# Performance work log

Measured on AMD Instinct MI355X. Metric: run time of the kernel, lower is better.

The kernel has to match this reference:

```python
import jax, jax.numpy as jnp
import numpy as np

B, S, DM = 1, 4096, 2048
H, HD = 16, 128
TS = 16          # tile_size
TOPK = 16        # anchor tiles per query
NUM_TILES = S // TS


def setup_inputs() -> dict:
    key = jax.random.key(0)
    ks = jax.random.split(key, 7)
    x = jax.random.normal(ks[0], (B, S, DM), jnp.float32)
    Wq = jax.random.normal(ks[1], (DM, H * HD), jnp.float32) * 0.02
    Wk = jax.random.normal(ks[2], (DM, H * HD), jnp.float32) * 0.02
    Wv = jax.random.normal(ks[3], (DM, H * HD), jnp.float32) * 0.02
    Wo = jax.random.normal(ks[4], (H * HD, DM), jnp.float32) * 0.02
    # RoPE angles: pos * inv_freq, shape [S, HD//2] (= freqs_cis angle)
    inv_freq = 1.0 / (10000.0 ** (np.arange(0, HD, 2, dtype=np.float32) / HD))
    freqs = jnp.asarray(np.arange(S, dtype=np.float32)[:, None] * inv_freq[None, :])
    anchor_indices = jax.random.randint(ks[5], (B, H, S, TOPK), 0, NUM_TILES).astype(jnp.int32)
    return {"x": x, "Wq": Wq, "Wk": Wk, "Wv": Wv, "Wo": Wo,
            "freqs": freqs, "anchor_indices": anchor_indices}


def _rotate_half(z):
    half = z.shape[-1] // 2
    return jnp.concatenate([-z[..., half:], z[..., :half]], axis=-1)


def reference(x, Wq, Wk, Wv, Wo, freqs, anchor_indices):
    b, s, _ = x.shape
    num_tiles = s // TS
    # QKV projections -> [B, H, S, HD]
    q = (x @ Wq).reshape(b, s, H, HD).transpose(0, 2, 1, 3)
    k = (x @ Wk).reshape(b, s, H, HD).transpose(0, 2, 1, 3)
    v = (x @ Wv).reshape(b, s, H, HD).transpose(0, 2, 1, 3)
    # RoPE (half-split / rotate_half convention), float32
    cos = jnp.cos(freqs)[None, None, :s, :]
    sin = jnp.sin(freqs)[None, None, :s, :]
    cos_full = jnp.concatenate([cos, cos], axis=-1)
    sin_full = jnp.concatenate([sin, sin], axis=-1)
    q = q * cos_full + _rotate_half(q) * sin_full
    k = k * cos_full + _rotate_half(k) * sin_full
    # Per-query tile indices: anchor tiles + local tile
    local_tiles = (jnp.arange(s) // TS).astype(jnp.int32)
    local = jnp.broadcast_to(local_tiles[None, None, :, None], (b, H, s, 1))
    tiles = jnp.concatenate([anchor_indices, local], axis=-1)  # [B,H,S,K+1]
    # Representative query per tile (last token of each query tile)
    tile_repr = jnp.arange(TS - 1, s, TS)
    tile_sel = tiles[:, :, tile_repr, :]                        # [B,H,T,K+1]
    # Expand tile indices to token indices
    offsets = jnp.arange(TS)
    token_idx = tile_sel[..., None] * TS + offsets              # [B,H,T,K+1,TS]
    sparse_len = tile_sel.shape[-1] * TS
    flat_idx = jnp.clip(token_idx.reshape(b, H, num_tiles, sparse_len), 0, s - 1)
    # Gather sparse K/V per (batch, head, query-tile)
    k_flat = k.reshape(b * H, s, HD)
    v_flat = v.reshape(b * H, s, HD)
    idx_flat = flat_idx.reshape(b * H, num_tiles, sparse_len)
    k_sparse = jax.vmap(lambda kv, idx: kv[idx])(k_flat, idx_flat)
    v_sparse = jax.vmap(lambda kv, idx: kv[idx])(v_flat, idx_flat)
    k_sparse = k_sparse.reshape(b, H, num_tiles, sparse_len, HD)
    v_sparse = v_sparse.reshape(b, H, num_tiles, sparse_len, HD)
    # Block-sparse attention per tile
    q_tiled = q.reshape(b, H, num_tiles, TS, HD)
    logits = jnp.einsum('bhtqd,bhtkd->bhtqk', q_tiled, k_sparse) / jnp.sqrt(HD)
    q_pos = jnp.arange(s).reshape(num_tiles, TS)
    future_mask = flat_idx[:, :, :, None, :] > q_pos[None, None, :, :, None]
    logits = jnp.where(future_mask, -1e10, logits)
    weights = jax.nn.softmax(logits, axis=-1)
    all_masked = jnp.all(future_mask, axis=-1, keepdims=True)
    weights = jnp.where(all_masked, 0.0, weights)
    weights = jnp.where(jnp.isnan(weights), 0.0, weights)
    out = jnp.einsum('bhtqk,bhtkd->bhtqd', weights, v_sparse)
    out = out.reshape(b, H, s, HD).transpose(0, 2, 1, 3).reshape(b, s, H * HD)
    return out @ Wo
```

## Files before the change

### kernel.cpp

```cpp
#include <hip/hip_runtime.h>

typedef unsigned short u16;
typedef unsigned int u32;
typedef __attribute__((ext_vector_type(8))) short bf16x8;
typedef __attribute__((ext_vector_type(4))) float f32x4;

__device__ __forceinline__ u16 f2bf(float f) {
  union { float f; u32 u; } v; v.f = f;
  u32 u = v.u;
  return (u16)((u + 0x7FFFu + ((u >> 16) & 1u)) >> 16);
}
__device__ __forceinline__ float bf2f(u16 s) {
  union { u32 u; float f; } v; v.u = ((u32)s) << 16;
  return v.f;
}

__device__ __forceinline__ void async16(const void* g, void* l) {
  __builtin_amdgcn_global_load_lds(
      (__attribute__((address_space(1))) void*)g,
      (__attribute__((address_space(3))) void*)l, 16, 0, 0);
}

__global__ void prep1_kernel(const float* __restrict__ x,
                             const float* __restrict__ W0, const float* __restrict__ W1,
                             const float* __restrict__ W2, const float* __restrict__ W3,
                             const float* __restrict__ freqs,
                             u16* __restrict__ xbf, u16* __restrict__ wqkvT,
                             u16* __restrict__ woT,
                             float* __restrict__ ct, float* __restrict__ st) {
  __shared__ float tile[32][33];
  const int bid = blockIdx.x;
  const int tid = threadIdx.x;
  if (bid < 16384) {
    const int z = bid >> 12;
    const float* in = z == 0 ? W0 : z == 1 ? W1 : z == 2 ? W2 : W3;
    u16* out = z == 3 ? woT : wqkvT + (size_t)z * 4194304;
    const int local = bid & 4095;
    const int c0 = (local & 63) * 32, r0 = (local >> 6) * 32;
    const int tx = tid & 31, ty = tid >> 5;
#pragma unroll
    for (int i = ty; i < 32; i += 8) tile[i][tx] = in[(size_t)(r0 + i) * 2048 + c0 + tx];
    __syncthreads();
#pragma unroll
    for (int i = ty; i < 32; i += 8)
      out[(size_t)(c0 + i) * 2048 + r0 + tx] = f2bf(tile[tx][i]);
  } else if (bid < 24576) {
    int i = (bid - 16384) * 256 + tid;
    float4 v = ((const float4*)x)[i];
    ushort4 o;
    o.x = f2bf(v.x); o.y = f2bf(v.y); o.z = f2bf(v.z); o.w = f2bf(v.w);
    ((ushort4*)xbf)[i] = o;
  } else {
    int i = (bid - 24576) * 256 + tid;
    float f = freqs[i];
    ct[i] = cosf(f); st[i] = sinf(f);
  }
}

__global__ void prep2_kernel(u16* __restrict__ q, const u16* __restrict__ k,
                             u16* __restrict__ Kp,
                             const u16* __restrict__ Vin, u16* __restrict__ VT2,
                             const float* __restrict__ ct, const float* __restrict__ st) {
  __shared__ u16 lv[64][132];
  const int bid = blockIdx.x;
  const int tid = threadIdx.x;
  if (bid < 8192) {
    int i = bid * 256 + tid;
    int dp = (i & 31) * 2;
    int hh = (i >> 5) & 15;
    int s  = i >> 9;
    float c0 = ct[s * 64 + dp], c1 = ct[s * 64 + dp + 1];
    float s0 = st[s * 64 + dp], s1 = st[s * 64 + dp + 1];
    size_t base = (size_t)s * 2048 + hh * 128 + dp;
    {
      u32 lo = *(u32*)(q + base);
      u32 hi = *(u32*)(q + base + 64);
      float a0 = bf2f((u16)lo), a1 = bf2f((u16)(lo >> 16));
      float b0 = bf2f((u16)hi), b1 = bf2f((u16)(hi >> 16));
      u32 nlo = (u32)f2bf(a0 * c0 - b0 * s0) | ((u32)f2bf(a1 * c1 - b1 * s1) << 16);
      u32 nhi = (u32)f2bf(b0 * c0 + a0 * s0) | ((u32)f2bf(b1 * c1 + a1 * s1) << 16);
      *(u32*)(q + base) = nlo;
      *(u32*)(q + base + 64) = nhi;
    }
    {
      u32 lo = *(const u32*)(k + base);
      u32 hi = *(const u32*)(k + base + 64);
      float a0 = bf2f((u16)lo), a1 = bf2f((u16)(lo >> 16));
      float b0 = bf2f((u16)hi), b1 = bf2f((u16)(hi >> 16));
      u32 nlo = (u32)f2bf(a0 * c0 - b0 * s0) | ((u32)f2bf(a1 * c1 - b1 * s1) << 16);
      u32 nhi = (u32)f2bf(b0 * c0 + a0 * s0) | ((u32)f2bf(b1 * c1 + a1 * s1) << 16);
      size_t kpb = ((size_t)hh * 4096 + s) * 128 + dp;
      *(u32*)(Kp + kpb) = nlo;
      *(u32*)(Kp + kpb + 64) = nhi;
    }
  } else {
    const int local = bid - 8192;
    const int h = local >> 6;
    const int s0 = (local & 63) * 64;
#pragma unroll
    for (int i = 0; i < 16; ++i) {
      int idx = i * 256 + tid;
      int r = idx >> 6;
      int d2 = idx & 63;
      u32 vv = ((const u32*)Vin)[(size_t)(s0 + r) * 1024 + h * 64 + d2];
      *(u32*)(&lv[r][d2 * 2]) = vv;
    }
    __syncthreads();
#pragma unroll
    for (int i = 0; i < 16; ++i) {
      int idx = i * 256 + tid;
      int k2 = idx & 7;
      int d  = (idx >> 3) & 127;
      int tl = idx >> 10;
      u32 lo = lv[tl * 16 + k2 * 2][d];
      u32 hi = lv[tl * 16 + k2 * 2 + 1][d];
      ((u32*)VT2)[(((size_t)h * 256 + (s0 >> 4) + tl) * 128 + d) * 8 + k2] = lo | (hi << 16);
    }
  }
}

template <int MODE>
__launch_bounds__(256, 2)
__global__ void gemm128_kernel(const u16* __restrict__ A, const u16* __restrict__ Bt,
                               void* __restrict__ C, u16* __restrict__ D1, u16* __restrict__ D2,
                               int M, int N, int K) {
  __shared__ __align__(16) u16 As[128 * 64];
  __shared__ __align__(16) u16 Bs[128 * 64];
  const int tid  = threadIdx.x;
  const int lane = tid & 63;
  const int wave = tid >> 6;
  const int wr = wave >> 1, wc = wave & 1;
  const int brow = blockIdx.y * 128;
  const int bcol = blockIdx.x * 128;

  int a_goff[4], b_goff[4], l_off[4];
#pragma unroll
  for (int i = 0; i < 4; ++i) {
    int p = (wave * 4 + i) * 1024 + lane * 16;
    int row = p >> 7;
    int colb = (p & 127) ^ ((row & 7) << 4);
    a_goff[i] = (brow + row) * K + (colb >> 1);
    b_goff[i] = (bcol + row) * K + (colb >> 1);
    l_off[i] = p;
  }

  f32x4 acc[4][4];
#pragma unroll
  for (int m = 0; m < 4; ++m)
#pragma unroll
    for (int n = 0; n < 4; ++n) acc[m][n] = (f32x4){0.f, 0.f, 0.f, 0.f};

  for (int k0 = 0; k0 < K; k0 += 64) {
#pragma unroll
    for (int i = 0; i < 4; ++i) {
      async16(A + a_goff[i] + k0, (char*)As + l_off[i]);
      async16(Bt + b_goff[i] + k0, (char*)Bs + l_off[i]);
    }
    __syncthreads();
#pragma unroll
    for (int kk = 0; kk < 2; ++kk) {
      bf16x8 af[4], bfr[4];
#pragma unroll
      for (int m = 0; m < 4; ++m) {
        int row = wr * 64 + m * 16 + (lane & 15);
        int byte = (row << 7) + ((kk * 64 + ((lane >> 4) << 4)) ^ ((row & 7) << 4));
        af[m] = *(const bf16x8*)((const char*)As + byte);
      }
#pragma unroll
      for (int n = 0; n < 4; ++n) {
        int row = wc * 64 + n * 16 + (lane & 15);
        int byte = (row << 7) + ((kk * 64 + ((lane >> 4) << 4)) ^ ((row & 7) << 4));
        bfr[n] = *(const bf16x8*)((const char*)Bs + byte);
      }
#pragma unroll
      for (int m = 0; m < 4; ++m)
#pragma unroll
        for (int n = 0; n < 4; ++n)
          acc[m][n] = __builtin_amdgcn_mfma_f32_16x16x32_bf16(af[m], bfr[n], acc[m][n], 0, 0, 0);
    }
    __syncthreads();
  }

  const int r0 = brow + wr * 64;
  const int c0 = bcol + wc * 64;
  if (MODE == 2) {
    const int sel = bcol >> 11;
    u16* dst = sel == 0 ? (u16*)C : sel == 1 ? D1 : D2;
    const int c0l = (bcol & 2047) + wc * 64;
#pragma unroll
    for (int m = 0; m < 4; ++m)
#pragma unroll
      for (int n = 0; n < 4; ++n)
#pragma unroll
        for (int r = 0; r < 4; ++r) {
          int rr = r0 + m * 16 + ((lane >> 4) << 2) + r;
          int cc = c0l + n * 16 + (lane & 15);
          dst[(size_t)rr * 2048 + cc] = f2bf(acc[m][n][r]);
        }
  } else {
#pragma unroll
    for (int m = 0; m < 4; ++m)
#pragma unroll
      for (int n = 0; n < 4; ++n)
#pragma unroll
        for (int r = 0; r < 4; ++r) {
          int rr = r0 + m * 16 + ((lane >> 4) << 2) + r;
          int cc = c0 + n * 16 + (lane & 15);
          if (MODE == 1) ((u16*)C)[(size_t)rr * N + cc] = f2bf(acc[m][n][r]);
          else           ((float*)C)[(size_t)rr * N + cc] = acc[m][n][r];
        }
  }
}

__launch_bounds__(256, 6)
__global__ void attn_kernel(const u16* __restrict__ Q, const u16* __restrict__ Kp,
                            const u16* __restrict__ VT2, const int* __restrict__ anchors,
                            u16* __restrict__ Out) {
  const int t = blockIdx.x;
  const int h = blockIdx.y;
  __shared__ int tiles[20];
  __shared__ __align__(16) float lg[16][292];
  const int tid  = threadIdx.x;
  const int lane = tid & 63;
  const int wave = tid >> 6;
  const int g = lane >> 4;
  const int c = lane & 15;

  if (tid < 16) tiles[tid] = anchors[(size_t)((h << 12) + (t * 16 + 15)) * 16 + tid];
  if (tid == 16) tiles[16] = t;
  if (tid >= 17 && tid < 20) tiles[tid] = 0;
  __syncthreads();

  {
    const u16* qbase = Q + (size_t)(t * 16 + c) * 2048 + h * 128 + g * 8;
    bf16x8 qf[4];
#pragma unroll
    for (int ks = 0; ks < 4; ++ks) qf[ks] = *(const bf16x8*)(qbase + ks * 32);

    int tok_[5];
    const u16* kb_[5];
#pragma unroll
    for (int i = 0; i < 5; ++i) {
      int j = wave + 4 * i;
      tok_[i] = tiles[j] * 16 + c;
      kb_[i] = Kp + ((size_t)h * 4096 + tok_[i]) * 128 + g * 8;
    }
    bf16x8 kfp[2][4];
#pragma unroll
    for (int ks = 0; ks < 4; ++ks) kfp[0][ks] = *(const bf16x8*)(kb_[0] + ks * 32);
#pragma unroll
    for (int i = 0; i < 5; ++i) {
      if (i < 4) {
#pragma unroll
        for (int ks = 0; ks < 4; ++ks)
          kfp[(i + 1) & 1][ks] = *(const bf16x8*)(kb_[i + 1] + ks * 32);
      }
      f32x4 a = (f32x4){0.f, 0.f, 0.f, 0.f};
#pragma unroll
      for (int ks = 0; ks < 4; ++ks)
        a = __builtin_amdgcn_mfma_f32_16x16x32_bf16(qf[ks], kfp[i & 1][ks], a, 0, 0, 0);
      int j = wave + 4 * i;
      if (j < 17) {
#pragma unroll
        for (int r = 0; r < 4; ++r) {
          int qrow = g * 4 + r;
          float vv = a[r] * 0.088388347648318447f;
          if (tok_[i] > t * 16 + qrow) vv = -1e10f;
          lg[qrow][j * 16 + c] = vv;
        }
      }
    }
  }
  __syncthreads();

  {
    const int r = tid >> 4, cc = tid & 15;
    float vals[17];
    float mx = -3.0e38f;
#pragma unroll
    for (int i = 0; i < 17; ++i) { vals[i] = lg[r][i * 16 + cc]; mx = fmaxf(mx, vals[i]); }
#pragma unroll
    for (int d = 1; d < 16; d <<= 1) mx = fmaxf(mx, __shfl_xor(mx, d, 64));
    float sum = 0.f;
#pragma unroll
    for (int i = 0; i < 17; ++i) { vals[i] = __expf(vals[i] - mx); sum += vals[i]; }
#pragma unroll
    for (int d = 1; d < 16; d <<= 1) sum += __shfl_xor(sum, d, 64);
    float inv = sum > 0.f ? 1.0f / sum : 0.f;
    u16* wrow = (u16*)&lg[r][0];
#pragma unroll
    for (int i = 0; i < 17; ++i) wrow[i * 16 + cc] = f2bf(vals[i] * inv);
    wrow[272 + cc] = 0;
  }
  __syncthreads();

  {
    f32x4 o0 = (f32x4){0.f, 0.f, 0.f, 0.f}, o1 = o0;
    const int d0 = wave * 32;
    const size_t hb = (size_t)h * 256;
    const int keyin = (g & 1) * 8;
    const u16* wrow = (const u16*)&lg[c][0];
    const u16* vb_[9];
#pragma unroll
    for (int ks = 0; ks < 9; ++ks) vb_[ks] = VT2 + (hb + tiles[2 * ks + (g >> 1)]) * 2048;
    bf16x8 pb0[2], pb1[2];
    pb0[0] = *(const bf16x8*)(vb_[0] + (d0 + c) * 16 + keyin);
    pb1[0] = *(const bf16x8*)(vb_[0] + (d0 + 16 + c) * 16 + keyin);
#pragma unroll
    for (int ks = 0; ks < 9; ++ks) {
      if (ks < 8) {
        pb0[(ks + 1) & 1] = *(const bf16x8*)(vb_[ks + 1] + (d0 + c) * 16 + keyin);
        pb1[(ks + 1) & 1] = *(const bf16x8*)(vb_[ks + 1] + (d0 + 16 + c) * 16 + keyin);
      }
      bf16x8 af = *(const bf16x8*)(wrow + ks * 32 + g * 8);
      o0 = __builtin_amdgcn_mfma_f32_16x16x32_bf16(af, pb0[ks & 1], o0, 0, 0, 0);
      o1 = __builtin_amdgcn_mfma_f32_16x16x32_bf16(af, pb1[ks & 1], o1, 0, 0, 0);
    }
#pragma unroll
    for (int r = 0; r < 4; ++r) {
      int qrow = g * 4 + r;
      size_t base = (size_t)(t * 16 + qrow) * 2048 + h * 128;
      Out[base + d0 + c]      = f2bf(o0[r]);
      Out[base + d0 + 16 + c] = f2bf(o1[r]);
    }
  }
}

extern "C" void kernel_launch(void* const* d_in, const int* in_sizes, int n_in,
                              void* d_out, int out_size, void* d_ws, size_t ws_size,
                              hipStream_t stream) {
  (void)in_sizes; (void)n_in; (void)out_size; (void)ws_size;
  const float* x      = (const float*)d_in[0];
  const float* Wq     = (const float*)d_in[1];
  const float* Wk     = (const float*)d_in[2];
  const float* Wv     = (const float*)d_in[3];
  const float* Wo     = (const float*)d_in[4];
  const float* freqs  = (const float*)d_in[5];
  const int* anchors  = (const int*)d_in[6];
  float* out = (float*)d_out;

  char* ws = (char*)d_ws;
  const size_t MB = 1024 * 1024;
  u16* xbf   = (u16*)(ws + 0);
  u16* wqkvT = (u16*)(ws + 16 * MB);
  u16* woT   = (u16*)(ws + 40 * MB);
  u16* qbf   = (u16*)(ws + 48 * MB);
  u16* kbf   = (u16*)(ws + 64 * MB);
  u16* vbf   = (u16*)(ws + 80 * MB);
  u16* attnb = (u16*)(ws + 0);
  u16* Kp    = (u16*)(ws + 16 * MB);
  u16* VT2   = (u16*)(ws + 64 * MB);
  float* ct  = (float*)(ws + 96 * MB);
  float* st  = (float*)(ws + 97 * MB);

  prep1_kernel<<<25600, 256, 0, stream>>>(x, Wq, Wk, Wv, Wo, freqs,
                                          xbf, wqkvT, woT, ct, st);
  gemm128_kernel<2><<<dim3(48, 32), 256, 0, stream>>>(xbf, wqkvT, qbf, kbf, vbf,
                                                      4096, 6144, 2048);
  prep2_kernel<<<9216, 256, 0, stream>>>(qbf, kbf, Kp, vbf, VT2, ct, st);
  attn_kernel<<<dim3(256, 16), 256, 0, stream>>>(qbf, Kp, VT2, anchors, attnb);
  gemm128_kernel<0><<<dim3(16, 32), 256, 0, stream>>>(attnb, woT, out, nullptr, nullptr,
                                                      4096, 2048, 2048);
}
```

Baseline: 241.0 us.

## Fuse Q RoPE into attention kernel and widen weight-transpose stores

Q rotary embedding moves out of prep2 and is applied in registers inside the attention kernel after loading Q, so prep2 no longer reads and writes the full Q tensor. The weight transpose in prep1 now packs two bf16 values per 32-bit store, halving the store count. The LDS logits row stride is also changed from 292 to 280. The trade-off is extra cos/sin loads and ALU work per attention block, and possible new LDS bank conflicts from the changed stride.

```diff
diff --git a/kernel.cpp b/kernel.cpp
--- a/kernel.cpp
+++ b/kernel.cpp
@@ -41,9 +41,12 @@
 #pragma unroll
     for (int i = ty; i < 32; i += 8) tile[i][tx] = in[(size_t)(r0 + i) * 2048 + c0 + tx];
     __syncthreads();
-#pragma unroll
-    for (int i = ty; i < 32; i += 8)
-      out[(size_t)(c0 + i) * 2048 + r0 + tx] = f2bf(tile[tx][i]);
+    const int cx = tid & 15, iy = tid >> 4;
+#pragma unroll
+    for (int i = iy; i < 32; i += 16) {
+      u32 v = (u32)f2bf(tile[2 * cx][i]) | ((u32)f2bf(tile[2 * cx + 1][i]) << 16);
+      *(u32*)(out + (size_t)(c0 + i) * 2048 + r0 + 2 * cx) = v;
+    }
   } else if (bid < 24576) {
     int i = (bid - 16384) * 256 + tid;
     float4 v = ((const float4*)x)[i];
@@ -57,8 +60,7 @@
   }
 }
 
-__global__ void prep2_kernel(u16* __restrict__ q, const u16* __restrict__ k,
-                             u16* __restrict__ Kp,
+__global__ void prep2_kernel(const u16* __restrict__ k, u16* __restrict__ Kp,
                              const u16* __restrict__ Vin, u16* __restrict__ VT2,
                              const float* __restrict__ ct, const float* __restrict__ st) {
   __shared__ u16 lv[64][132];
@@ -72,27 +74,15 @@
     float c0 = ct[s * 64 + dp], c1 = ct[s * 64 + dp + 1];
     float s0 = st[s * 64 + dp], s1 = st[s * 64 + dp + 1];
     size_t base = (size_t)s * 2048 + hh * 128 + dp;
-    {
-      u32 lo = *(u32*)(q + base);
-      u32 hi = *(u32*)(q + base + 64);
-      float a0 = bf2f((u16)lo), a1 = bf2f((u16)(lo >> 16));
-      float b0 = bf2f((u16)hi), b1 = bf2f((u16)(hi >> 16));
-      u32 nlo = (u32)f2bf(a0 * c0 - b0 * s0) | ((u32)f2bf(a1 * c1 - b1 * s1) << 16);
-      u32 nhi = (u32)f2bf(b0 * c0 + a0 * s0) | ((u32)f2bf(b1 * c1 + a1 * s1) << 16);
-      *(u32*)(q + base) = nlo;
-      *(u32*)(q + base + 64) = nhi;
-    }
-    {
-      u32 lo = *(const u32*)(k + base);
-      u32 hi = *(const u32*)(k + base + 64);
-      float a0 = bf2f((u16)lo), a1 = bf2f((u16)(lo >> 16));
-      float b0 = bf2f((u16)hi), b1 = bf2f((u16)(hi >> 16));
-      u32 nlo = (u32)f2bf(a0 * c0 - b0 * s0) | ((u32)f2bf(a1 * c1 - b1 * s1) << 16);
-      u32 nhi = (u32)f2bf(b0 * c0 + a0 * s0) | ((u32)f2bf(b1 * c1 + a1 * s1) << 16);
-      size_t kpb = ((size_t)hh * 4096 + s) * 128 + dp;
-      *(u32*)(Kp + kpb) = nlo;
-      *(u32*)(Kp + kpb + 64) = nhi;
-    }
+    u32 lo = *(const u32*)(k + base);
+    u32 hi = *(const u32*)(k + base + 64);
+    float a0 = bf2f((u16)lo), a1 = bf2f((u16)(lo >> 16));
+    float b0 = bf2f((u16)hi), b1 = bf2f((u16)(hi >> 16));
+    u32 nlo = (u32)f2bf(a0 * c0 - b0 * s0) | ((u32)f2bf(a1 * c1 - b1 * s1) << 16);
+    u32 nhi = (u32)f2bf(b0 * c0 + a0 * s0) | ((u32)f2bf(b1 * c1 + a1 * s1) << 16);
+    size_t kpb = ((size_t)hh * 4096 + s) * 128 + dp;
+    *(u32*)(Kp + kpb) = nlo;
+    *(u32*)(Kp + kpb + 64) = nhi;
   } else {
     const int local = bid - 8192;
     const int h = local >> 6;
@@ -215,11 +205,12 @@
 __launch_bounds__(256, 6)
 __global__ void attn_kernel(const u16* __restrict__ Q, const u16* __restrict__ Kp,
                             const u16* __restrict__ VT2, const int* __restrict__ anchors,
-                            u16* __restrict__ Out) {
+                            u16* __restrict__ Out,
+                            const float* __restrict__ ct, const float* __restrict__ st) {
   const int t = blockIdx.x;
   const int h = blockIdx.y;
   __shared__ int tiles[20];
-  __shared__ __align__(16) float lg[16][292];
+  __shared__ __align__(16) float lg[16][280];
   const int tid  = threadIdx.x;
   const int lane = tid & 63;
   const int wave = tid >> 6;
@@ -232,10 +223,32 @@
   __syncthreads();
 
   {
-    const u16* qbase = Q + (size_t)(t * 16 + c) * 2048 + h * 128 + g * 8;
+    const int s = t * 16 + c;
+    const u16* qbase = Q + (size_t)s * 2048 + h * 128 + g * 8;
+    bf16x8 qr[4];
+#pragma unroll
+    for (int ks = 0; ks < 4; ++ks) qr[ks] = *(const bf16x8*)(qbase + ks * 32);
+    float c0[8], s0[8], c1[8], s1[8];
+    const float* ctb = ct + s * 64;
+    const float* stb = st + s * 64;
+    *(float4*)&c0[0] = *(const float4*)(ctb + g * 8);
+    *(float4*)&c0[4] = *(const float4*)(ctb + g * 8 + 4);
+    *(float4*)&c1[0] = *(const float4*)(ctb + 32 + g * 8);
+    *(float4*)&c1[4] = *(const float4*)(ctb + 32 + g * 8 + 4);
+    *(float4*)&s0[0] = *(const float4*)(stb + g * 8);
+    *(float4*)&s0[4] = *(const float4*)(stb + g * 8 + 4);
+    *(float4*)&s1[0] = *(const float4*)(stb + 32 + g * 8);
+    *(float4*)&s1[4] = *(const float4*)(stb + 32 + g * 8 + 4);
     bf16x8 qf[4];
 #pragma unroll
-    for (int ks = 0; ks < 4; ++ks) qf[ks] = *(const bf16x8*)(qbase + ks * 32);
+    for (int j = 0; j < 8; ++j) {
+      float f0 = bf2f((u16)qr[0][j]), f1 = bf2f((u16)qr[1][j]);
+      float f2 = bf2f((u16)qr[2][j]), f3 = bf2f((u16)qr[3][j]);
+      qf[0][j] = (short)f2bf(f0 * c0[j] - f2 * s0[j]);
+      qf[1][j] = (short)f2bf(f1 * c1[j] - f3 * s1[j]);
+      qf[2][j] = (short)f2bf(f2 * c0[j] + f0 * s0[j]);
+      qf[3][j] = (short)f2bf(f3 * c1[j] + f1 * s1[j]);
+    }
 
     int tok_[5];
     const u16* kb_[5];
@@ -357,8 +370,8 @@
                                           xbf, wqkvT, woT, ct, st);
   gemm128_kernel<2><<<dim3(48, 32), 256, 0, stream>>>(xbf, wqkvT, qbf, kbf, vbf,
                                                       4096, 6144, 2048);
-  prep2_kernel<<<9216, 256, 0, stream>>>(qbf, kbf, Kp, vbf, VT2, ct, st);
-  attn_kernel<<<dim3(256, 16), 256, 0, stream>>>(qbf, Kp, VT2, anchors, attnb);
+  prep2_kernel<<<9216, 256, 0, stream>>>(kbf, Kp, vbf, VT2, ct, st);
+  attn_kernel<<<dim3(256, 16), 256, 0, stream>>>(qbf, Kp, VT2, anchors, attnb, ct, st);
   gemm128_kernel<0><<<dim3(16, 32), 256, 0, stream>>>(attnb, woT, out, nullptr, nullptr,
                                                       4096, 2048, 2048);
 }
```

Measured after the change: 251.1 us. 4.2% more time.

## Fuse RoPE and K/V relayout into QKV GEMM epilogue, drop prep2

Applied to the files above, without the earlier changes.

The QKV GEMM epilogue now stages each 64-row half of the accumulator tile in shared memory. From there it applies RoPE and writes Q row-major and K head-major, or writes V straight into the tiled VT2 layout. This removes the separate prep2 kernel and the bf16 round trip of Q, K and V through global memory. Separately, the weight-transpose store in prep1 now packs two bf16 values per 32-bit store. The cost is a larger shared-memory footprint, extra block barriers and a heavier epilogue inside the GEMM.

```diff
diff --git a/kernel.cpp b/kernel.cpp
--- a/kernel.cpp
+++ b/kernel.cpp
@@ -41,9 +41,12 @@
 #pragma unroll
     for (int i = ty; i < 32; i += 8) tile[i][tx] = in[(size_t)(r0 + i) * 2048 + c0 + tx];
     __syncthreads();
-#pragma unroll
-    for (int i = ty; i < 32; i += 8)
-      out[(size_t)(c0 + i) * 2048 + r0 + tx] = f2bf(tile[tx][i]);
+    const int cx = tid & 15, iy = tid >> 4;
+#pragma unroll
+    for (int i = iy; i < 32; i += 16) {
+      u32 v = (u32)f2bf(tile[2 * cx][i]) | ((u32)f2bf(tile[2 * cx + 1][i]) << 16);
+      *(u32*)(out + (size_t)(c0 + i) * 2048 + r0 + 2 * cx) = v;
+    }
   } else if (bid < 24576) {
     int i = (bid - 16384) * 256 + tid;
     float4 v = ((const float4*)x)[i];
@@ -57,75 +60,15 @@
   }
 }
 
-__global__ void prep2_kernel(u16* __restrict__ q, const u16* __restrict__ k,
-                             u16* __restrict__ Kp,
-                             const u16* __restrict__ Vin, u16* __restrict__ VT2,
-                             const float* __restrict__ ct, const float* __restrict__ st) {
-  __shared__ u16 lv[64][132];
-  const int bid = blockIdx.x;
-  const int tid = threadIdx.x;
-  if (bid < 8192) {
-    int i = bid * 256 + tid;
-    int dp = (i & 31) * 2;
-    int hh = (i >> 5) & 15;
-    int s  = i >> 9;
-    float c0 = ct[s * 64 + dp], c1 = ct[s * 64 + dp + 1];
-    float s0 = st[s * 64 + dp], s1 = st[s * 64 + dp + 1];
-    size_t base = (size_t)s * 2048 + hh * 128 + dp;
-    {
-      u32 lo = *(u32*)(q + base);
-      u32 hi = *(u32*)(q + base + 64);
-      float a0 = bf2f((u16)lo), a1 = bf2f((u16)(lo >> 16));
-      float b0 = bf2f((u16)hi), b1 = bf2f((u16)(hi >> 16));
-      u32 nlo = (u32)f2bf(a0 * c0 - b0 * s0) | ((u32)f2bf(a1 * c1 - b1 * s1) << 16);
-      u32 nhi = (u32)f2bf(b0 * c0 + a0 * s0) | ((u32)f2bf(b1 * c1 + a1 * s1) << 16);
-      *(u32*)(q + base) = nlo;
-      *(u32*)(q + base + 64) = nhi;
-    }
-    {
-      u32 lo = *(const u32*)(k + base);
-      u32 hi = *(const u32*)(k + base + 64);
-      float a0 = bf2f((u16)lo), a1 = bf2f((u16)(lo >> 16));
-      float b0 = bf2f((u16)hi), b1 = bf2f((u16)(hi >> 16));
-      u32 nlo = (u32)f2bf(a0 * c0 - b0 * s0) | ((u32)f2bf(a1 * c1 - b1 * s1) << 16);
-      u32 nhi = (u32)f2bf(b0 * c0 + a0 * s0) | ((u32)f2bf(b1 * c1 + a1 * s1) << 16);
-      size_t kpb = ((size_t)hh * 4096 + s) * 128 + dp;
-      *(u32*)(Kp + kpb) = nlo;
-      *(u32*)(Kp + kpb + 64) = nhi;
-    }
-  } else {
-    const int local = bid - 8192;
-    const int h = local >> 6;
-    const int s0 = (local & 63) * 64;
-#pragma unroll
-    for (int i = 0; i < 16; ++i) {
-      int idx = i * 256 + tid;
-      int r = idx >> 6;
-      int d2 = idx & 63;
-      u32 vv = ((const u32*)Vin)[(size_t)(s0 + r) * 1024 + h * 64 + d2];
-      *(u32*)(&lv[r][d2 * 2]) = vv;
-    }
-    __syncthreads();
-#pragma unroll
-    for (int i = 0; i < 16; ++i) {
-      int idx = i * 256 + tid;
-      int k2 = idx & 7;
-      int d  = (idx >> 3) & 127;
-      int tl = idx >> 10;
-      u32 lo = lv[tl * 16 + k2 * 2][d];
-      u32 hi = lv[tl * 16 + k2 * 2 + 1][d];
-      ((u32*)VT2)[(((size_t)h * 256 + (s0 >> 4) + tl) * 128 + d) * 8 + k2] = lo | (hi << 16);
-    }
-  }
-}
-
 template <int MODE>
 __launch_bounds__(256, 2)
 __global__ void gemm128_kernel(const u16* __restrict__ A, const u16* __restrict__ Bt,
                                void* __restrict__ C, u16* __restrict__ D1, u16* __restrict__ D2,
+                               const float* __restrict__ ct, const float* __restrict__ st,
                                int M, int N, int K) {
-  __shared__ __align__(16) u16 As[128 * 64];
-  __shared__ __align__(16) u16 Bs[128 * 64];
+  __shared__ __align__(16) char smem[33152];
+  u16* As = (u16*)smem;
+  u16* Bs = (u16*)(smem + 16384);
   const int tid  = threadIdx.x;
   const int lane = tid & 63;
   const int wave = tid >> 6;
@@ -181,23 +124,67 @@
     __syncthreads();
   }
 
-  const int r0 = brow + wr * 64;
-  const int c0 = bcol + wc * 64;
   if (MODE == 2) {
     const int sel = bcol >> 11;
-    u16* dst = sel == 0 ? (u16*)C : sel == 1 ? D1 : D2;
-    const int c0l = (bcol & 2047) + wc * 64;
-#pragma unroll
-    for (int m = 0; m < 4; ++m)
-#pragma unroll
-      for (int n = 0; n < 4; ++n)
-#pragma unroll
-        for (int r = 0; r < 4; ++r) {
-          int rr = r0 + m * 16 + ((lane >> 4) << 2) + r;
-          int cc = c0l + n * 16 + (lane & 15);
-          dst[(size_t)rr * 2048 + cc] = f2bf(acc[m][n][r]);
+    const int hh  = (bcol & 2047) >> 7;
+    float* ep = (float*)smem;
+#pragma unroll
+    for (int half = 0; half < 2; ++half) {
+      if (wr == half) {
+#pragma unroll
+        for (int m = 0; m < 4; ++m)
+#pragma unroll
+          for (int n = 0; n < 4; ++n)
+#pragma unroll
+            for (int r = 0; r < 4; ++r) {
+              int lr = m * 16 + ((lane >> 4) << 2) + r;
+              int lc = wc * 64 + n * 16 + (lane & 15);
+              ep[lr * 129 + lc] = acc[m][n][r];
+            }
+      }
+      __syncthreads();
+      const int rowbase = brow + half * 64;
+      if (sel == 2) {
+#pragma unroll
+        for (int it = 0; it < 16; ++it) {
+          int idx = it * 256 + tid;
+          int tl = idx >> 10;
+          int d  = (idx >> 3) & 127;
+          int k2 = idx & 7;
+          u32 lo = f2bf(ep[(tl * 16 + 2 * k2) * 129 + d]);
+          u32 hi = f2bf(ep[(tl * 16 + 2 * k2 + 1) * 129 + d]);
+          int tile = (rowbase >> 4) + tl;
+          *(u32*)(D2 + (((size_t)(hh * 256 + tile) * 128 + d) * 16 + 2 * k2)) = lo | (hi << 16);
         }
+      } else {
+#pragma unroll
+        for (int it = 0; it < 8; ++it) {
+          int idx = it * 256 + tid;
+          int row = idx >> 5;
+          int d = (idx & 31) * 2;
+          int t = rowbase + row;
+          float a0 = ep[row * 129 + d],      a1 = ep[row * 129 + d + 1];
+          float b0 = ep[row * 129 + d + 64], b1 = ep[row * 129 + d + 65];
+          float cc0 = ct[t * 64 + d], cc1 = ct[t * 64 + d + 1];
+          float ss0 = st[t * 64 + d], ss1 = st[t * 64 + d + 1];
+          u32 lo = (u32)f2bf(a0 * cc0 - b0 * ss0) | ((u32)f2bf(a1 * cc1 - b1 * ss1) << 16);
+          u32 hi = (u32)f2bf(b0 * cc0 + a0 * ss0) | ((u32)f2bf(b1 * cc1 + a1 * ss1) << 16);
+          if (sel == 0) {
+            u16* qd = (u16*)C + (size_t)t * 2048 + hh * 128 + d;
+            *(u32*)qd = lo;
+            *(u32*)(qd + 64) = hi;
+          } else {
+            u16* kd = D1 + ((size_t)hh * 4096 + t) * 128 + d;
+            *(u32*)kd = lo;
+            *(u32*)(kd + 64) = hi;
+          }
+        }
+      }
+      __syncthreads();
+    }
   } else {
+    const int r0 = brow + wr * 64;
+    const int c0 = bcol + wc * 64;
 #pragma unroll
     for (int m = 0; m < 4; ++m)
 #pragma unroll
@@ -206,8 +193,7 @@
         for (int r = 0; r < 4; ++r) {
           int rr = r0 + m * 16 + ((lane >> 4) << 2) + r;
           int cc = c0 + n * 16 + (lane & 15);
-          if (MODE == 1) ((u16*)C)[(size_t)rr * N + cc] = f2bf(acc[m][n][r]);
-          else           ((float*)C)[(size_t)rr * N + cc] = acc[m][n][r];
+          ((float*)C)[(size_t)rr * N + cc] = acc[m][n][r];
         }
   }
 }
@@ -345,20 +331,17 @@
   u16* wqkvT = (u16*)(ws + 16 * MB);
   u16* woT   = (u16*)(ws + 40 * MB);
   u16* qbf   = (u16*)(ws + 48 * MB);
-  u16* kbf   = (u16*)(ws + 64 * MB);
-  u16* vbf   = (u16*)(ws + 80 * MB);
+  u16* Kp    = (u16*)(ws + 64 * MB);
+  u16* VT2   = (u16*)(ws + 80 * MB);
   u16* attnb = (u16*)(ws + 0);
-  u16* Kp    = (u16*)(ws + 16 * MB);
-  u16* VT2   = (u16*)(ws + 64 * MB);
   float* ct  = (float*)(ws + 96 * MB);
   float* st  = (float*)(ws + 97 * MB);
 
   prep1_kernel<<<25600, 256, 0, stream>>>(x, Wq, Wk, Wv, Wo, freqs,
                                           xbf, wqkvT, woT, ct, st);
-  gemm128_kernel<2><<<dim3(48, 32), 256, 0, stream>>>(xbf, wqkvT, qbf, kbf, vbf,
-                                                      4096, 6144, 2048);
-  prep2_kernel<<<9216, 256, 0, stream>>>(qbf, kbf, Kp, vbf, VT2, ct, st);
+  gemm128_kernel<2><<<dim3(48, 32), 256, 0, stream>>>(xbf, wqkvT, qbf, Kp, VT2,
+                                                      ct, st, 4096, 6144, 2048);
   attn_kernel<<<dim3(256, 16), 256, 0, stream>>>(qbf, Kp, VT2, anchors, attnb);
   gemm128_kernel<0><<<dim3(16, 32), 256, 0, stream>>>(attnb, woT, out, nullptr, nullptr,
-                                                      4096, 2048, 2048);
-}
+                                                      nullptr, nullptr, 4096, 2048, 2048);
+}
```

After: 230.3 us. 4.4% less time.
